# Kernel optimization log

Measured on AMD Instinct MI355X. Metric: run time of the kernel, lower is better.

Reference implementation:

```python
import jax, jax.numpy as jnp
import numpy as np
from jax import lax

B, C, H, W = 4, 256, 64, 64
O = 256
EPS = 1e-5


def setup_inputs() -> dict:
    key = jax.random.key(0)
    ks = jax.random.split(key, 20)
    s = 0.02
    d = {
        'input1': jax.random.normal(ks[0], (B, C, H, W), jnp.float32),
        'input2': jax.random.normal(ks[1], (B, C, H, W), jnp.float32),
        'wq1': jax.random.normal(ks[2], (C // 8, C), jnp.float32) * s,
        'bq1': jnp.zeros((C // 8,), jnp.float32),
        'wk1': jax.random.normal(ks[3], (C // 4, C), jnp.float32) * s,
        'bk1': jnp.zeros((C // 4,), jnp.float32),
        'wv1': jax.random.normal(ks[4], (C, C), jnp.float32) * s,
        'bv1': jnp.zeros((C,), jnp.float32),
        'wq2': jax.random.normal(ks[5], (C // 8, C), jnp.float32) * s,
        'bq2': jnp.zeros((C // 8,), jnp.float32),
        'wk2': jax.random.normal(ks[6], (C // 4, C), jnp.float32) * s,
        'bk2': jnp.zeros((C // 4,), jnp.float32),
        'wv2': jax.random.normal(ks[7], (C, C), jnp.float32) * s,
        'bv2': jnp.zeros((C,), jnp.float32),
        'gamma': jnp.asarray([0.1], jnp.float32),
        'w_cat': jax.random.normal(ks[8], (O, 2 * C, 3, 3), jnp.float32) * s,
        'bn_scale': jnp.ones((O,), jnp.float32),
        'bn_bias': jnp.zeros((O,), jnp.float32),
        'bn_mean': jnp.zeros((O,), jnp.float32),
        'bn_var': jnp.ones((O,), jnp.float32),
    }
    return d


def _conv1x1(x, w, b):
    # x: [B,C,H,W], w: [Co,C] -> [B,Co,H,W]
    return jnp.einsum('bchw,oc->bohw', x, w) + b[None, :, None, None]


def reference(input1, input2, wq1, bq1, wk1, bk1, wv1, bv1,
              wq2, bq2, wk2, bk2, wv2, bv2, gamma, w_cat,
              bn_scale, bn_bias, bn_mean, bn_var):
    b, c, h, w = input1.shape
    hw = h * w
    q1 = _conv1x1(input1, wq1, bq1)
    k1 = _conv1x1(input1, wk1, bk1).reshape(b, -1, hw)
    v1 = _conv1x1(input1, wv1, bv1).reshape(b, -1, hw)
    q2 = _conv1x1(input2, wq2, bq2)
    k2 = _conv1x1(input2, wk2, bk2).reshape(b, -1, hw)
    v2 = _conv1x1(input2, wv2, bv2).reshape(b, -1, hw)
    # concat q heads along channel -> [B, C/4, HW] -> [B, HW, C/4]
    q = jnp.concatenate([q1, q2], axis=1).reshape(b, -1, hw).transpose(0, 2, 1)
    # branch 1: [B,HW,HW] scores (no scaling, as in source)
    attn1 = jax.nn.softmax(jnp.einsum('bnc,bcm->bnm', q, k1), axis=-1)
    out1 = jnp.einsum('bcm,bnm->bcn', v1, attn1).reshape(b, c, h, w)
    out1 = gamma[0] * out1 + input1
    # branch 2
    attn2 = jax.nn.softmax(jnp.einsum('bnc,bcm->bnm', q, k2), axis=-1)
    out2 = jnp.einsum('bcm,bnm->bcn', v2, attn2).reshape(b, c, h, w)
    out2 = gamma[0] * out2 + input2
    # conv_cat: 3x3 conv (no bias) + BatchNorm (eval stats) + ReLU
    cat = jnp.concatenate([out1, out2], axis=1)
    conv = lax.conv_general_dilated(cat, w_cat, (1, 1), 'SAME',
                                    dimension_numbers=('NCHW', 'OIHW', 'NCHW'))
    inv = bn_scale / jnp.sqrt(bn_var + EPS)
    bn = conv * inv[None, :, None, None] + (bn_bias - bn_mean * inv)[None, :, None, None]
    feat_sum = jax.nn.relu(bn)
    return (feat_sum, out1, out2)
```

## Files before the change

### kernel.cpp

```cpp
#include <hip/hip_runtime.h>
#include <hip/hip_bf16.h>

#define HW 4096

#define KT_OFF   1048576
#define WTP_OFF  1572864
#define O1_OFF   4194304
#define WVB_OFF  1179648
#define XBF_OFF  1310720
#define WS_NEED  19398656ull

typedef short v8s  __attribute__((ext_vector_type(8)));
typedef float v16f __attribute__((ext_vector_type(16)));

#define LSTR 72
#define ZSTR 264
#define CPAD 20
#define PL_ROWS 128
#define PL_SZ  (2 * PL_ROWS * LSTR)
#define XP_SZ  (2 * 256 * LSTR)
#define XLHALF (4 * 66 * CPAD)

__device__ __forceinline__ unsigned short f2b(float f) {
    unsigned u = __float_as_uint(f);
    return (unsigned short)((u + 0x7fffu + ((u >> 16) & 1u)) >> 16);
}
__device__ __forceinline__ unsigned cvt_pk_bf16(float lo, float hi) {
    float2 f2; f2.x = lo; f2.y = hi;
    __hip_bfloat162 h = __float22bfloat162_rn(f2);
    unsigned r;
    __builtin_memcpy(&r, &h, 4);
    return r;
}
__device__ __forceinline__ v8s load8(const unsigned short* p) {
    union { uint2 u[2]; v8s v; } t;
    t.u[0] = *(const uint2*)p;
    t.u[1] = *(const uint2*)(p + 4);
    return t.v;
}

__global__ __launch_bounds__(256) void wprep_proj(
    const float* __restrict__ wq1, const float* __restrict__ wk1, const float* __restrict__ wv1,
    const float* __restrict__ wq2, const float* __restrict__ wk2, const float* __restrict__ wv2,
    float* __restrict__ wtp) {
    int idx = blockIdx.x * 256 + threadIdx.x;
    if (idx >= 2 * 256 * 352) return;
    int sel = idx / 90112;
    int r   = idx - sel * 90112;
    int c   = r / 352;
    int co  = r - c * 352;
    const float* w; int row;
    if (co < 32)      { w = sel ? wq2 : wq1; row = co; }
    else if (co < 96) { w = sel ? wk2 : wk1; row = co - 32; }
    else              { w = sel ? wv2 : wv1; row = co - 96; }
    wtp[idx] = w[row * 256 + c];
}

__global__ __launch_bounds__(256) void wprep_convw(const float* __restrict__ wcat,
                                                   unsigned short* __restrict__ wt) {
    int i = blockIdx.x * 256 + threadIdx.x;
    if (i >= 32 * 9 * 256 * 16) return;
    const int ci_l = i & 15;
    const int o    = (i >> 4) & 255;
    const int t2   = i >> 12;
    const int tap  = t2 % 9;
    const int chunk = t2 / 9;
    wt[i] = f2b(wcat[((size_t)o * 512 + chunk * 16 + ci_l) * 9 + tap]);
}

__global__ __launch_bounds__(256) void wprep_wv(const float* __restrict__ wv1,
                                                const float* __restrict__ wv2,
                                                unsigned short* __restrict__ out) {
    int i = blockIdx.x * 256 + threadIdx.x;
    if (i >= 131072) return;
    const float* src = (i < 65536) ? wv1 : wv2;
    out[i] = f2b(src[i & 65535]);
}

__global__ __launch_bounds__(256) void wprep_xbf(const float* __restrict__ x1,
                                                 const float* __restrict__ x2,
                                                 unsigned short* __restrict__ xbf) {
    const size_t e = ((size_t)blockIdx.x * 256 + threadIdx.x) * 8;
    if (e >= 8388608) return;
    const float* src = (e < 4194304) ? (x1 + e) : (x2 + (e - 4194304));
    const float4 a = *(const float4*)src;
    const float4 c = *(const float4*)(src + 4);
    uint4 o;
    o.x = cvt_pk_bf16(a.x, a.y); o.y = cvt_pk_bf16(a.z, a.w);
    o.z = cvt_pk_bf16(c.x, c.y); o.w = cvt_pk_bf16(c.z, c.w);
    *(uint4*)&xbf[e] = o;
}

__global__ __launch_bounds__(256) void proj_kernel(
    const float* __restrict__ x1, const float* __restrict__ x2,
    const float* __restrict__ bq1, const float* __restrict__ bk1,
    const float* __restrict__ bq2, const float* __restrict__ bk2,
    float* __restrict__ dout) {
    __shared__ __align__(16) float xls[256][64];
    const int tile = blockIdx.x, sel = blockIdx.y, b = blockIdx.z;
    const int n0 = tile * 64;
    const float* xb = (sel ? x2 : x1) + (size_t)b * 256 * HW;

    for (int i = threadIdx.x; i < 4096; i += 256) {
        const int row = i >> 4, c4 = (i & 15) * 4;
        *(float4*)&xls[row][c4] = *(const float4*)(xb + (size_t)row * HW + n0 + c4);
    }
    __syncthreads();

    const int n   = threadIdx.x & 63;
    const int cog = __builtin_amdgcn_readfirstlane(threadIdx.x >> 6);
    const float* bq = sel ? bq2 : bq1;
    const float* bk = sel ? bk2 : bk1;
    const float* wc = dout + WTP_OFF + (size_t)sel * 90112;
    unsigned short* qtg = (unsigned short*)dout + (size_t)b * HW * 64;
    unsigned short* ktg = (unsigned short*)dout + KT_OFF + (size_t)(sel * 4 + b) * HW * 64;

    for (int blk = 0; blk < 3; ++blk) {
        const int co0 = cog * 24 + blk * 8;
        float acc[8];
        const float* brow; int r0; bool isq;
        if (co0 < 32) { r0 = co0;      brow = bq; isq = true;  }
        else          { r0 = co0 - 32; brow = bk; isq = false; }
        #pragma unroll
        for (int k = 0; k < 8; ++k) acc[k] = brow[r0 + k];
        #pragma unroll 4
        for (int c = 0; c < 256; ++c) {
            const float xv = xls[c][n];
            const float4 w0 = *(const float4*)(wc + (size_t)c * 352 + co0);
            const float4 w1 = *(const float4*)(wc + (size_t)c * 352 + co0 + 4);
            acc[0] += xv * w0.x; acc[1] += xv * w0.y; acc[2] += xv * w0.z; acc[3] += xv * w0.w;
            acc[4] += xv * w1.x; acc[5] += xv * w1.y; acc[6] += xv * w1.z; acc[7] += xv * w1.w;
        }
        unsigned pk2[4];
        #pragma unroll
        for (int k = 0; k < 4; ++k) pk2[k] = cvt_pk_bf16(acc[2 * k], acc[2 * k + 1]);
        unsigned short* dst = isq ? (qtg + (size_t)(n0 + n) * 64 + sel * 32 + r0)
                                  : (ktg + (size_t)(n0 + n) * 64 + r0);
        *(uint4*)dst = *(const uint4*)pk2;
    }
}

template <int USEBF>
__global__ __launch_bounds__(512, 2) void attn_kernel(
    const float* __restrict__ in1, const float* __restrict__ in2,
    const unsigned short* __restrict__ xbf,
    const unsigned short* __restrict__ wvbf,
    const float* __restrict__ bv1, const float* __restrict__ bv2,
    const float* __restrict__ gamma_p,
    float* __restrict__ dout) {
    __shared__ __align__(16) unsigned short smem[PL_SZ + XP_SZ];
    __shared__ float rsums[128][2];
    __shared__ float lfin[128];

    const int bid = blockIdx.x;
    const int g   = bid & 7;
    const int qt  = bid >> 3;
    const int br  = g >> 2, b = g & 3;
    const int t = threadIdx.x;
    const int w = t >> 6, lane = t & 63, h = lane >> 5, l32 = lane & 31;

    const unsigned short* qtg = (const unsigned short*)dout + (size_t)b * HW * 64;
    const unsigned short* ktg = (const unsigned short*)dout + KT_OFF + (size_t)(br * 4 + b) * HW * 64;
    const float* xg = (br ? in2 : in1) + (size_t)b * 256 * HW;
    float* zo = dout + O1_OFF + (size_t)br * 4194304 + (size_t)b * 256 * HW;

    const int msub = (w & 1) * 32;
    const int nsub = (w >> 1) * 32;
    const int cs   = w & 3;
    const int nh   = w >> 2;
    const int koff = h * 8;

    unsigned short* plds = smem;
    unsigned short* xp   = smem + PL_SZ;

    v8s aq[4];
    #pragma unroll
    for (int ks = 0; ks < 4; ++ks)
        aq[ks] = *(const v8s*)(qtg + (size_t)(qt * 128 + nsub + l32) * 64 + ks * 16 + koff);

    const unsigned short* kpt = ktg + (size_t)(msub + l32) * 64 + koff;
    v8s kf[4];
    #pragma unroll
    for (int ks = 0; ks < 4; ++ks)
        kf[ks] = *(const v8s*)(kpt + ks * 16);

    const int m4 = (t & 15) * 4, r0i = t >> 4;
    const float* xgp = xg + (size_t)r0i * HW + m4;
    const unsigned short* xbp = xbf + (size_t)br * 4194304
                              + (size_t)b * 256 * HW + (size_t)r0i * HW + m4;

    uint2 xpk[8];
    if constexpr (USEBF) {
        #pragma unroll
        for (int j = 0; j < 8; ++j) xpk[j] = *(const uint2*)(xbp + (size_t)j * 32 * HW);
    } else {
        float4 xr0[8];
        #pragma unroll
        for (int j = 0; j < 8; ++j) xr0[j] = *(const float4*)(xgp + (size_t)j * 32 * HW);
        #pragma unroll
        for (int j = 0; j < 8; ++j) {
            xpk[j].x = cvt_pk_bf16(xr0[j].x, xr0[j].y);
            xpk[j].y = cvt_pk_bf16(xr0[j].z, xr0[j].w);
        }
    }

    v16f a00, a01, a10, a11;
    #pragma unroll
    for (int i = 0; i < 16; ++i) { a00[i] = 0.f; a01[i] = 0.f; a10[i] = 0.f; a11[i] = 0.f; }
    float racc = 0.f;

    #pragma unroll 1
    for (int mt = 0; mt < 64; ++mt) {
        const int cur = mt & 1;
        v16f s;
        #pragma unroll
        for (int i = 0; i < 16; ++i) s[i] = 0.f;
        #pragma unroll
        for (int ks = 0; ks < 4; ++ks)
            s = __builtin_amdgcn_mfma_f32_32x32x16_bf16(kf[ks], aq[ks], s, 0, 0, 0);
        const int mg = (mt < 63) ? (mt + 1) * 64 : 0;
        #pragma unroll
        for (int ks = 0; ks < 4; ++ks)
            kf[ks] = *(const v8s*)(kpt + (size_t)mg * 64 + ks * 16);
        float4 xr[8];
        if constexpr (!USEBF) {
            #pragma unroll
            for (int j = 0; j < 8; ++j)
                xr[j] = *(const float4*)(xgp + (size_t)j * 32 * HW + mg);
        }
        unsigned short* prow = plds + (size_t)(cur * PL_ROWS + nsub + l32) * LSTR + msub;
        #pragma unroll
        for (int rp = 0; rp < 8; ++rp) {
            const float e0 = __expf(s[2 * rp]);
            const float e1 = __expf(s[2 * rp + 1]);
            racc += e0 + e1;
            const int m0 = ((2 * rp) & 3) + 8 * (rp >> 1) + 4 * h;
            *(unsigned*)&prow[m0] = cvt_pk_bf16(e0, e1);
        }
        {
            unsigned short* xw = xp + (size_t)(cur * 256 + r0i) * LSTR + m4;
            #pragma unroll
            for (int j = 0; j < 8; ++j)
                *(uint2*)(xw + (size_t)j * 32 * LSTR) = xpk[j];
        }
        if constexpr (USEBF) {
            #pragma unroll
            for (int j = 0; j < 8; ++j)
                xpk[j] = *(const uint2*)(xbp + (size_t)j * 32 * HW + mg);
        }
        __syncthreads();
        {
            const unsigned short* xb0 = xp + (size_t)(cur * 256 + cs * 64 + l32) * LSTR;
            const unsigned short* xb1 = xb0 + (size_t)32 * LSTR;
            const unsigned short* pb0 = plds + (size_t)(cur * PL_ROWS + nh * 64 + l32) * LSTR;
            const unsigned short* pb1 = pb0 + (size_t)32 * LSTR;
            #pragma unroll
            for (int ks = 0; ks < 4; ++ks) {
                const int mo = ks * 16 + koff;
                const v8s xa0 = *(const v8s*)(xb0 + mo);
                const v8s xa1 = *(const v8s*)(xb1 + mo);
                const v8s pf0 = *(const v8s*)(pb0 + mo);
                const v8s pf1 = *(const v8s*)(pb1 + mo);
                a00 = __builtin_amdgcn_mfma_f32_32x32x16_bf16(xa0, pf0, a00, 0, 0, 0);
                a01 = __builtin_amdgcn_mfma_f32_32x32x16_bf16(xa0, pf1, a01, 0, 0, 0);
                a10 = __builtin_amdgcn_mfma_f32_32x32x16_bf16(xa1, pf0, a10, 0, 0, 0);
                a11 = __builtin_amdgcn_mfma_f32_32x32x16_bf16(xa1, pf1, a11, 0, 0, 0);
            }
        }
        if constexpr (!USEBF) {
            #pragma unroll
            for (int j = 0; j < 8; ++j) {
                xpk[j].x = cvt_pk_bf16(xr[j].x, xr[j].y);
                xpk[j].y = cvt_pk_bf16(xr[j].z, xr[j].w);
            }
        }
    }
    __syncthreads();
    {
        const float rtot = racc + __shfl_xor(racc, 32);
        if (lane < 32) rsums[nsub + l32][w & 1] = rtot;
    }
    __syncthreads();
    if (t < 128) lfin[t] = 1.0f / (rsums[t][0] + rsums[t][1]);
    __syncthreads();
    const float dn0 = lfin[nh * 64 + l32];
    const float dn1 = lfin[nh * 64 + 32 + l32];
    unsigned short (*zt)[ZSTR] = (unsigned short (*)[ZSTR])smem;
    #pragma unroll
    for (int rp = 0; rp < 8; ++rp) {
        const int r = rp * 2;
        const int c = cs * 64 + (r & 3) + 8 * (r >> 2) + 4 * h;
        const int n0r = nh * 64 + l32, n1r = nh * 64 + 32 + l32;
        *(unsigned*)&zt[n0r][c]      = cvt_pk_bf16(a00[r] * dn0, a00[r + 1] * dn0);
        *(unsigned*)&zt[n1r][c]      = cvt_pk_bf16(a01[r] * dn1, a01[r + 1] * dn1);
        *(unsigned*)&zt[n0r][c + 32] = cvt_pk_bf16(a10[r] * dn0, a10[r + 1] * dn0);
        *(unsigned*)&zt[n1r][c + 32] = cvt_pk_bf16(a11[r] * dn1, a11[r + 1] * dn1);
    }
    __syncthreads();
    const unsigned short* wvb = wvbf + (size_t)br * 65536;
    const float* bvp = br ? bv2 : bv1;
    const float gamma = gamma_p[0];
    const int ob = cs * 64;
    const int ncol = qt * 128 + nh * 64;
    v16f m00, m01, m10, m11;
    #pragma unroll
    for (int i = 0; i < 16; ++i) { m00[i] = 0.f; m01[i] = 0.f; m10[i] = 0.f; m11[i] = 0.f; }
    #pragma unroll
    for (int ks = 0; ks < 16; ++ks) {
        const int k = ks * 16 + koff;
        const v8s aA = *(const v8s*)(wvb + (size_t)(ob + l32) * 256 + k);
        const v8s aB = *(const v8s*)(wvb + (size_t)(ob + 32 + l32) * 256 + k);
        const v8s b0v = *(const v8s*)&zt[nh * 64 + l32][k];
        const v8s b1v = *(const v8s*)&zt[nh * 64 + 32 + l32][k];
        m00 = __builtin_amdgcn_mfma_f32_32x32x16_bf16(aA, b0v, m00, 0, 0, 0);
        m01 = __builtin_amdgcn_mfma_f32_32x32x16_bf16(aA, b1v, m01, 0, 0, 0);
        m10 = __builtin_amdgcn_mfma_f32_32x32x16_bf16(aB, b0v, m10, 0, 0, 0);
        m11 = __builtin_amdgcn_mfma_f32_32x32x16_bf16(aB, b1v, m11, 0, 0, 0);
    }
    #pragma unroll
    for (int r = 0; r < 16; ++r) {
        const int o = ob + (r & 3) + 8 * (r >> 2) + 4 * h;
        const float bvA = bvp[o], bvB = bvp[o + 32];
        const size_t base0 = (size_t)o * HW + ncol;
        const size_t base1 = (size_t)(o + 32) * HW + ncol;
        zo[base0 + l32]      = gamma * (m00[r] + bvA) + xg[base0 + l32];
        zo[base0 + 32 + l32] = gamma * (m01[r] + bvA) + xg[base0 + 32 + l32];
        zo[base1 + l32]      = gamma * (m10[r] + bvB) + xg[base1 + l32];
        zo[base1 + 32 + l32] = gamma * (m11[r] + bvB) + xg[base1 + 32 + l32];
    }
}

__global__ __launch_bounds__(256) void conv_kernel(
    const unsigned short* __restrict__ wt,
    const float* __restrict__ bn_scale, const float* __restrict__ bn_bias,
    const float* __restrict__ bn_mean,  const float* __restrict__ bn_var,
    float* __restrict__ dout) {
    __shared__ __align__(16) unsigned short xl[2][4][66][CPAD];
    __shared__ __align__(16) unsigned short wl[2][9][64][CPAD];

    const int bid = blockIdx.x;
    const int xcd = bid & 7, j = bid >> 3;
    const int G   = xcd * 16 + (j >> 2);
    const int ot  = j & 3;
    const int pt  = G & 31;
    const int b   = G >> 5;
    const int h0 = pt * 2;
    const int t  = threadIdx.x;
    const int w  = t >> 6, lane = t & 63, h = lane >> 5, l32 = lane & 31;
    const int osub = (w & 1) * 32;
    const int ps0  = (w >> 1) * 64;

    int ldsoff[9], srcoff[9]; bool valid[9], inb[9];
    #pragma unroll
    for (int k = 0; k < 9; ++k) {
        const int i = t + k * 256;
        valid[k] = i < 2112;
        const int col = i % 66, rem = i / 66;
        const int row = rem & 3, cp = rem >> 2;
        const int hh = h0 + row - 1, ww = col - 1;
        inb[k] = (hh >= 0 && hh < 64 && ww >= 0 && ww < 64);
        srcoff[k] = 2 * cp * HW + (inb[k] ? hh * 64 + ww : 0);
        ldsoff[k] = (row * 66 + col) * CPAD + 2 * cp;
    }
    unsigned short* xlf = &xl[0][0][0][0];

    float inv[16], add[16];
    #pragma unroll
    for (int r = 0; r < 16; ++r) {
        const int o_g = ot * 64 + osub + (r & 3) + 8 * (r >> 2) + 4 * h;
        const float iv = bn_scale[o_g] * __frsqrt_rn(bn_var[o_g] + 1e-5f);
        inv[r] = iv;
        add[r] = bn_bias[o_g] - bn_mean[o_g] * iv;
    }

    v16f acc0, acc1;
    #pragma unroll
    for (int i = 0; i < 16; ++i) { acc0[i] = 0.f; acc1[i] = 0.f; }

    const float* bsrc = dout + O1_OFF + (size_t)b * 1048576;
    const unsigned short* wbase = wt + (size_t)(ot * 64) * 16;

    float xv0[9], xv1[9];
    uint2 wr[9];
    {
        const float* src = bsrc;
        #pragma unroll
        for (int k = 0; k < 9; ++k) {
            xv0[k] = 0.f; xv1[k] = 0.f;
            if (valid[k] && inb[k]) {
                const float* p = src + srcoff[k];
                xv0[k] = p[0]; xv1[k] = p[HW];
            }
        }
        #pragma unroll
        for (int u9 = 0; u9 < 9; ++u9) {
            const int u = t + u9 * 256;
            const int tap = u >> 8, rem2 = u & 255;
            const int o = rem2 >> 2, q = rem2 & 3;
            wr[u9] = *(const uint2*)(wbase + ((size_t)tap * 256 + o) * 16 + q * 4);
        }
    }

    #pragma unroll 1
    for (int chunk = 0; chunk < 32; ++chunk) {
        const int cur = chunk & 1;
        #pragma unroll
        for (int k = 0; k < 9; ++k)
            if (valid[k])
                *(unsigned*)&xlf[cur * XLHALF + ldsoff[k]] = cvt_pk_bf16(xv0[k], xv1[k]);
        #pragma unroll
        for (int u9 = 0; u9 < 9; ++u9) {
            const int u = t + u9 * 256;
            const int tap = u >> 8, rem2 = u & 255;
            const int o = rem2 >> 2, q = rem2 & 3;
            *(uint2*)&wl[cur][tap][o][q * 4] = wr[u9];
        }
        if (chunk < 31) {
            const int cn = chunk + 1;
            const float* src = bsrc + (size_t)(cn < 16 ? 0 : 1) * 4194304
                             + (size_t)((cn & 15) * 16) * HW;
            #pragma unroll
            for (int k = 0; k < 9; ++k) {
                xv0[k] = 0.f; xv1[k] = 0.f;
                if (valid[k] && inb[k]) {
                    const float* p = src + srcoff[k];
                    xv0[k] = p[0]; xv1[k] = p[HW];
                }
            }
            const unsigned short* wsl = wbase + (size_t)cn * 36864;
            #pragma unroll
            for (int u9 = 0; u9 < 9; ++u9) {
                const int u = t + u9 * 256;
                const int tap = u >> 8, rem2 = u & 255;
                const int o = rem2 >> 2, q = rem2 & 3;
                wr[u9] = *(const uint2*)(wsl + ((size_t)tap * 256 + o) * 16 + q * 4);
            }
        }
        __syncthreads();
        #pragma unroll
        for (int dy = 0; dy < 3; ++dy) {
            #pragma unroll
            for (int dx = 0; dx < 3; ++dx) {
                const v8s af = load8(&wl[cur][dy * 3 + dx][osub + l32][h * 8]);
                const int n0 = ps0 + l32, n1 = ps0 + 32 + l32;
                const v8s b0 = load8(&xl[cur][(n0 >> 6) + dy][(n0 & 63) + dx][h * 8]);
                const v8s b1 = load8(&xl[cur][(n1 >> 6) + dy][(n1 & 63) + dx][h * 8]);
                acc0 = __builtin_amdgcn_mfma_f32_32x32x16_bf16(af, b0, acc0, 0, 0, 0);
                acc1 = __builtin_amdgcn_mfma_f32_32x32x16_bf16(af, b1, acc1, 0, 0, 0);
            }
        }
    }
    const int px0 = ps0 + l32, px1 = ps0 + 32 + l32;
    const size_t gpx0 = (size_t)(h0 + (px0 >> 6)) * 64 + (px0 & 63);
    const size_t gpx1 = (size_t)(h0 + (px1 >> 6)) * 64 + (px1 & 63);
    #pragma unroll
    for (int r = 0; r < 16; ++r) {
        const int o_g = ot * 64 + osub + (r & 3) + 8 * (r >> 2) + 4 * h;
        const size_t obase = ((size_t)b * 256 + o_g) * HW;
        float v0 = acc0[r] * inv[r] + add[r];
        float v1 = acc1[r] * inv[r] + add[r];
        v0 = v0 > 0.f ? v0 : 0.f;
        v1 = v1 > 0.f ? v1 : 0.f;
        dout[obase + gpx0] = v0;
        dout[obase + gpx1] = v1;
    }
}

extern "C" void kernel_launch(void* const* d_in, const int* in_sizes, int n_in,
                              void* d_out, int out_size, void* d_ws, size_t ws_size,
                              hipStream_t stream) {
    (void)in_sizes; (void)n_in; (void)out_size;
    const float* x1   = (const float*)d_in[0];
    const float* x2   = (const float*)d_in[1];
    const float* wq1  = (const float*)d_in[2];
    const float* bq1  = (const float*)d_in[3];
    const float* wk1  = (const float*)d_in[4];
    const float* bk1  = (const float*)d_in[5];
    const float* wv1  = (const float*)d_in[6];
    const float* bv1  = (const float*)d_in[7];
    const float* wq2  = (const float*)d_in[8];
    const float* bq2  = (const float*)d_in[9];
    const float* wk2  = (const float*)d_in[10];
    const float* bk2  = (const float*)d_in[11];
    const float* wv2  = (const float*)d_in[12];
    const float* bv2  = (const float*)d_in[13];
    const float* gma  = (const float*)d_in[14];
    const float* wcat = (const float*)d_in[15];
    const float* bns  = (const float*)d_in[16];
    const float* bnb  = (const float*)d_in[17];
    const float* bnm  = (const float*)d_in[18];
    const float* bnv  = (const float*)d_in[19];

    float* out = (float*)d_out;
    unsigned short* wtc = (unsigned short*)d_ws;
    unsigned short* wvb = wtc + WVB_OFF;
    unsigned short* xbf = wtc + XBF_OFF;
    const bool use_bf = ws_size >= WS_NEED;

    wprep_proj<<<704, 256, 0, stream>>>(wq1, wk1, wv1, wq2, wk2, wv2, out + WTP_OFF);
    wprep_convw<<<4608, 256, 0, stream>>>(wcat, wtc);
    wprep_wv<<<512, 256, 0, stream>>>(wv1, wv2, wvb);
    if (use_bf) wprep_xbf<<<4096, 256, 0, stream>>>(x1, x2, xbf);
    proj_kernel<<<dim3(64, 2, 4), 256, 0, stream>>>(x1, x2, bq1, bk1, bq2, bk2, out);
    if (use_bf)
        attn_kernel<1><<<256, 512, 0, stream>>>(x1, x2, xbf, wvb, bv1, bv2, gma, out);
    else
        attn_kernel<0><<<256, 512, 0, stream>>>(x1, x2, xbf, wvb, bv1, bv2, gma, out);
    conv_kernel<<<512, 256, 0, stream>>>(wtc, bns, bnb, bnm, bnv, out);
}
```

Baseline: 402.7 us.

## Add padded bf16 copy of attention outputs and LDS-free MFMA conv kernel

Adds a pre-pass that converts out1/out2 into a zero-padded bf16 buffer laid out as 16-channel chunks, so the 3x3 conv can read its MFMA operands directly from global memory without boundary checks or LDS staging. The new conv kernel launches 1024 blocks of 32 output channels each, keeps one accumulator per wave, and applies BN+ReLU in the epilogue. The cost is an extra kernel launch and a full read/write pass over the activations, plus repeated uncached global loads for the tap neighbours. It is used only when the workspace is large enough; otherwise the old conv path runs.

```diff
diff --git a/kernel.cpp b/kernel.cpp
--- a/kernel.cpp
+++ b/kernel.cpp
@@ -9,6 +9,7 @@
 #define WVB_OFF  1179648
 #define XBF_OFF  1310720
 #define WS_NEED  19398656ull
+#define WS_NEED2 20463616ull
 
 typedef short v8s  __attribute__((ext_vector_type(8)));
 typedef float v16f __attribute__((ext_vector_type(16)));
@@ -20,6 +21,8 @@
 #define PL_SZ  (2 * PL_ROWS * LSTR)
 #define XP_SZ  (2 * 256 * LSTR)
 #define XLHALF (4 * 66 * CPAD)
+#define CPYCH  69696
+#define CPYB   2230272
 
 __device__ __forceinline__ unsigned short f2b(float f) {
     unsigned u = __float_as_uint(f);
@@ -327,6 +330,91 @@
         zo[base0 + 32 + l32] = gamma * (m01[r] + bvA) + xg[base0 + 32 + l32];
         zo[base1 + l32]      = gamma * (m10[r] + bvB) + xg[base1 + l32];
         zo[base1 + 32 + l32] = gamma * (m11[r] + bvB) + xg[base1 + 32 + l32];
+    }
+}
+
+__global__ __launch_bounds__(256) void cpy_pad(const float* __restrict__ dsrc,
+                                               unsigned short* __restrict__ cpy) {
+    __shared__ float xls[16][65];
+    const int hp = blockIdx.x, chunk = blockIdx.y, b = blockIdx.z;
+    const int t = threadIdx.x;
+    unsigned short* crow = cpy + (((size_t)(b * 32 + chunk) * 66 + hp) * 66) * 16;
+    if (hp == 0 || hp == 65) {
+        if (t < 132) *(uint4*)(crow + t * 8) = make_uint4(0, 0, 0, 0);
+        return;
+    }
+    const int hh = hp - 1;
+    const float* src = dsrc + O1_OFF + (size_t)(chunk < 16 ? 0 : 1) * 4194304
+                     + (size_t)b * 1048576 + (size_t)((chunk & 15) * 16) * HW + (size_t)hh * 64;
+    {
+        const int ci = t >> 6, ww = t & 63;
+        #pragma unroll
+        for (int j = 0; j < 4; ++j)
+            xls[ci + 4 * j][ww] = src[(size_t)(ci + 4 * j) * HW + ww];
+    }
+    __syncthreads();
+    {
+        const int wwp = t >> 2, q = t & 3;
+        uint2 pk;
+        pk.x = cvt_pk_bf16(xls[q * 4 + 0][wwp], xls[q * 4 + 1][wwp]);
+        pk.y = cvt_pk_bf16(xls[q * 4 + 2][wwp], xls[q * 4 + 3][wwp]);
+        *(uint2*)(crow + (size_t)(wwp + 1) * 16 + q * 4) = pk;
+    }
+    if (t < 4) {
+        unsigned short* p = crow + (size_t)(t >> 1) * 65 * 16 + (t & 1) * 8;
+        *(uint4*)p = make_uint4(0, 0, 0, 0);
+    }
+}
+
+__global__ __launch_bounds__(256, 4) void conv_bf(
+    const unsigned short* __restrict__ wt,
+    const unsigned short* __restrict__ cpy,
+    const float* __restrict__ bn_scale, const float* __restrict__ bn_bias,
+    const float* __restrict__ bn_mean,  const float* __restrict__ bn_var,
+    float* __restrict__ dout) {
+    const int bid = blockIdx.x;
+    const int lin = (bid & 7) * 128 + (bid >> 3);
+    const int ot  = lin & 7;
+    const int g   = lin >> 3;
+    const int pt  = g & 31, b = g >> 5;
+    const int h0  = pt * 2;
+    const int t   = threadIdx.x;
+    const int w   = t >> 6, lane = t & 63, h = lane >> 5, l32 = lane & 31;
+    const int n   = w * 32 + l32;
+    const int r0  = n >> 6, c0 = n & 63;
+
+    const unsigned short* wb = wt + (size_t)(ot * 32 + l32) * 16 + h * 8;
+    const unsigned short* cb = cpy + (size_t)b * CPYB
+                             + (size_t)(h0 + r0) * 66 * 16 + (size_t)c0 * 16 + h * 8;
+
+    v16f acc;
+    #pragma unroll
+    for (int i = 0; i < 16; ++i) acc[i] = 0.f;
+
+    #pragma unroll 1
+    for (int chunk = 0; chunk < 32; ++chunk) {
+        const unsigned short* wc = wb + (size_t)chunk * 9 * 4096;
+        const unsigned short* cc = cb + (size_t)chunk * CPYCH;
+        v8s wf[9], xf[9];
+        #pragma unroll
+        for (int tap = 0; tap < 9; ++tap) {
+            const int dy = tap / 3, dx = tap % 3;
+            wf[tap] = *(const v8s*)(wc + (size_t)tap * 4096);
+            xf[tap] = *(const v8s*)(cc + (size_t)(dy * 66 + dx) * 16);
+        }
+        #pragma unroll
+        for (int tap = 0; tap < 9; ++tap)
+            acc = __builtin_amdgcn_mfma_f32_32x32x16_bf16(wf[tap], xf[tap], acc, 0, 0, 0);
+    }
+    const size_t gp = (size_t)(h0 + r0) * 64 + c0;
+    #pragma unroll
+    for (int r = 0; r < 16; ++r) {
+        const int o_g = ot * 32 + (r & 3) + 8 * (r >> 2) + 4 * h;
+        const float iv = bn_scale[o_g] * __frsqrt_rn(bn_var[o_g] + 1e-5f);
+        const float ad = bn_bias[o_g] - bn_mean[o_g] * iv;
+        float v = acc[r] * iv + ad;
+        v = v > 0.f ? v : 0.f;
+        dout[((size_t)b * 256 + o_g) * HW + gp] = v;
     }
 }
 
@@ -495,7 +583,8 @@
     unsigned short* wtc = (unsigned short*)d_ws;
     unsigned short* wvb = wtc + WVB_OFF;
     unsigned short* xbf = wtc + XBF_OFF;
-    const bool use_bf = ws_size >= WS_NEED;
+    const bool use_bf  = ws_size >= WS_NEED;
+    const bool use_cvb = ws_size >= WS_NEED2;
 
     wprep_proj<<<704, 256, 0, stream>>>(wq1, wk1, wv1, wq2, wk2, wv2, out + WTP_OFF);
     wprep_convw<<<4608, 256, 0, stream>>>(wcat, wtc);
@@ -506,5 +595,10 @@
         attn_kernel<1><<<256, 512, 0, stream>>>(x1, x2, xbf, wvb, bv1, bv2, gma, out);
     else
         attn_kernel<0><<<256, 512, 0, stream>>>(x1, x2, xbf, wvb, bv1, bv2, gma, out);
-    conv_kernel<<<512, 256, 0, stream>>>(wtc, bns, bnb, bnm, bnv, out);
-}
+    if (use_cvb) {
+        cpy_pad<<<dim3(66, 32, 4), 256, 0, stream>>>(out, xbf);
+        conv_bf<<<1024, 256, 0, stream>>>(wtc, xbf, bns, bnb, bnm, bnv, out);
+    } else {
+        conv_kernel<<<512, 256, 0, stream>>>(wtc, bns, bnb, bnm, bnv, out);
+    }
+}
```

Result: slower. 424.3 us (+5.4%).
